# Optimization experiments

Hardware: AMD Instinct MI355X
Metric: run time of the kernel (lower is better)

## Reference

```python
import jax, jax.numpy as jnp
import numpy as np

B, T, C = 4, 2048, 1024
H, D = 16, 64  # n_heads, head_dim; C == H*D

def setup_inputs() -> dict:
    key = jax.random.key(0)
    ks = jax.random.split(key, 6)
    s_in = 1.0 / np.sqrt(C)
    x = jax.random.normal(ks[0], (B, T, C), dtype=jnp.float32)
    # causal mask: True above the diagonal -> masked to -inf
    mask = jnp.triu(jnp.ones((T, T), dtype=bool), k=1)
    Wqkv = jax.random.uniform(ks[1], (C, 3 * C), jnp.float32, -s_in, s_in)
    bqkv = jax.random.uniform(ks[2], (3 * C,), jnp.float32, -s_in, s_in)
    Wout = jax.random.uniform(ks[3], (C, C), jnp.float32, -s_in, s_in)
    bout = jax.random.uniform(ks[4], (C,), jnp.float32, -s_in, s_in)
    return {"x": x, "mask": mask, "Wqkv": Wqkv, "bqkv": bqkv, "Wout": Wout, "bout": bout}

def reference(x, mask, Wqkv, bqkv, Wout, bout):
    b, t, c = x.shape
    qkv = (x @ Wqkv + bqkv).reshape(b, t, 3, H, D)
    qkv = jnp.transpose(qkv, (2, 0, 3, 1, 4))  # [3, B, H, T, D]
    q, k, v = qkv[0], qkv[1], qkv[2]
    scores = jnp.einsum("bhqd,bhkd->bhqk", q, k) / jnp.sqrt(jnp.float32(D))
    scores = jnp.where(mask[:t, :t][None, None, :, :], -jnp.inf, scores)
    attn = jax.nn.softmax(scores, axis=-1)
    out = jnp.einsum("bhqk,bhkd->bhqd", attn, v)
    out = jnp.transpose(out, (0, 2, 1, 3)).reshape(b, t, c)
    return out @ Wout + bout
```

## Files before the change

### kernel.cpp

```cpp
#include <hip/hip_runtime.h>

typedef unsigned short u16;
typedef __attribute__((ext_vector_type(8))) short bf16x8;
typedef __attribute__((ext_vector_type(4))) short bf16x4;
typedef __attribute__((ext_vector_type(4))) float f32x4;

#define MFMA16(a, b, c) __builtin_amdgcn_mfma_f32_16x16x32_bf16(a, b, c, 0, 0, 0)

__device__ __forceinline__ u16 f2bf(float x) {
    unsigned u = __float_as_uint(x);
    return (u16)((u + 0x7fffu + ((u >> 16) & 1u)) >> 16);
}

__global__ __launch_bounds__(256) void castk(const float* __restrict__ src, u16* __restrict__ dst) {
    const int i = (blockIdx.x * 256 + threadIdx.x) * 8;
    float4 a = *(const float4*)(src + i);
    float4 b = *(const float4*)(src + i + 4);
    bf16x8 v;
    v[0] = (short)f2bf(a.x); v[1] = (short)f2bf(a.y);
    v[2] = (short)f2bf(a.z); v[3] = (short)f2bf(a.w);
    v[4] = (short)f2bf(b.x); v[5] = (short)f2bf(b.y);
    v[6] = (short)f2bf(b.z); v[7] = (short)f2bf(b.w);
    *(bf16x8*)(dst + i) = v;
}

__global__ __launch_bounds__(256) void tkern(const float* __restrict__ src, u16* __restrict__ dst,
                                             int R, int C) {
    const int tC = C >> 6;
    const int tr = (blockIdx.x / tC) << 6;
    const int tc = (blockIdx.x % tC) << 6;
    __shared__ u16 ls[64 * 68];
    const int tid = threadIdx.x;
#pragma unroll
    for (int rep = 0; rep < 2; ++rep) {
        const int f = tid * 8 + rep * 2048;
        const int r = f >> 6, c = f & 63;
        float4 a = *(const float4*)(src + (size_t)(tr + r) * C + tc + c);
        float4 b = *(const float4*)(src + (size_t)(tr + r) * C + tc + c + 4);
        bf16x4 lo, hi;
        lo[0] = (short)f2bf(a.x); lo[1] = (short)f2bf(a.y);
        lo[2] = (short)f2bf(a.z); lo[3] = (short)f2bf(a.w);
        hi[0] = (short)f2bf(b.x); hi[1] = (short)f2bf(b.y);
        hi[2] = (short)f2bf(b.z); hi[3] = (short)f2bf(b.w);
        *(bf16x4*)&ls[r * 68 + c] = lo;
        *(bf16x4*)&ls[r * 68 + c + 4] = hi;
    }
    __syncthreads();
#pragma unroll
    for (int rep = 0; rep < 2; ++rep) {
        const int f = tid * 8 + rep * 2048;
        const int rn = f >> 6, ck = f & 63;
        bf16x8 v;
#pragma unroll
        for (int j = 0; j < 8; ++j) v[j] = (short)ls[(ck + j) * 68 + rn];
        *(bf16x8*)(dst + (size_t)(tc + rn) * R + tr + ck) = v;
    }
}

template <int MODE>
__global__ __launch_bounds__(256) void gemm_k(const u16* __restrict__ A, const u16* __restrict__ Bt,
                                              const float* __restrict__ bias,
                                              u16* __restrict__ Qo, u16* __restrict__ Ko,
                                              u16* __restrict__ Vo, float* __restrict__ Of) {
    constexpr int Kd = 1024;
    const int tid = threadIdx.x;
    const int lane = tid & 63, wave = tid >> 6;
    const int wm = wave >> 1, wn = wave & 1;
    const int lr = lane & 15, lg = lane >> 4;
    const int mt = blockIdx.x & 63;
    const int nt = blockIdx.x >> 6;
    const int mbase = mt << 7, nbase = nt << 7;
    __shared__ u16 As[128 * 32];
    __shared__ u16 Bs[128 * 32];
    f32x4 acc[4][4];
#pragma unroll
    for (int i = 0; i < 4; ++i)
#pragma unroll
        for (int j = 0; j < 4; ++j) acc[i][j] = {0.f, 0.f, 0.f, 0.f};

    for (int kb = 0; kb < Kd; kb += 32) {
        __syncthreads();
#pragma unroll
        for (int rep = 0; rep < 2; ++rep) {
            const int f = tid * 8 + rep * 2048;
            const int r = f >> 5, c = f & 31;
            __builtin_amdgcn_global_load_lds(
                (const __attribute__((address_space(1))) void*)(A + (size_t)(mbase + r) * Kd + kb + c),
                (__attribute__((address_space(3))) void*)(As + f), 16, 0, 0);
            __builtin_amdgcn_global_load_lds(
                (const __attribute__((address_space(1))) void*)(Bt + (size_t)(nbase + r) * Kd + kb + c),
                (__attribute__((address_space(3))) void*)(Bs + f), 16, 0, 0);
        }
        __syncthreads();
        bf16x8 af[4], bfr[4];
#pragma unroll
        for (int i = 0; i < 4; ++i)
            af[i] = *(const bf16x8*)&As[(wm * 64 + i * 16 + lr) * 32 + lg * 8];
#pragma unroll
        for (int j = 0; j < 4; ++j)
            bfr[j] = *(const bf16x8*)&Bs[(wn * 64 + j * 16 + lr) * 32 + lg * 8];
#pragma unroll
        for (int i = 0; i < 4; ++i)
#pragma unroll
            for (int j = 0; j < 4; ++j) acc[i][j] = MFMA16(af[i], bfr[j], acc[i][j]);
    }

    const float QSCALE = 0.1803368801111137f;
#pragma unroll
    for (int j = 0; j < 4; ++j) {
        const int n = nbase + wn * 64 + j * 16 + lr;
        const float bj = bias[n];
        if (MODE == 0) {
            const int three = n >> 10;
            const int h = (n >> 6) & 15;
            const int d = n & 63;
#pragma unroll
            for (int i = 0; i < 4; ++i) {
#pragma unroll
                for (int r = 0; r < 4; ++r) {
                    const int m = mbase + wm * 64 + i * 16 + lg * 4 + r;
                    const int b = m >> 11, t = m & 2047;
                    const int bh = (b << 4) + h;
                    const float val = acc[i][j][r] + bj;
                    if (three == 0)
                        Qo[(((size_t)bh << 11) + t) * 64 + d] = f2bf(val * QSCALE);
                    else if (three == 1)
                        Ko[(((size_t)bh << 11) + t) * 64 + d] = f2bf(val);
                    else
                        Vo[(((size_t)bh << 6) + d) * 2048 + t] = f2bf(val);
                }
            }
        } else {
#pragma unroll
            for (int i = 0; i < 4; ++i) {
#pragma unroll
                for (int r = 0; r < 4; ++r) {
                    const int m = mbase + wm * 64 + i * 16 + lg * 4 + r;
                    Of[((size_t)m << 10) + n] = acc[i][j][r] + bj;
                }
            }
        }
    }
}

__global__ __launch_bounds__(256) void flash_attn(const u16* __restrict__ Q, const u16* __restrict__ Kg,
                                                  const u16* __restrict__ Vt, u16* __restrict__ Aout) {
    const int tid = threadIdx.x;
    const int lane = tid & 63, wave = tid >> 6;
    const int lr = lane & 15, lg = lane >> 4;
    const int qb = blockIdx.x;
    const int bh = blockIdx.y;
    const int b = bh >> 4, h = bh & 15;
    const size_t base = (size_t)bh << 17;

    __shared__ u16 Ks[64 * 72];
    __shared__ u16 Vs[64 * 72];
    __shared__ u16 Ps[4][16 * 72];

    const u16* Qrow = Q + base + (size_t)(qb * 64 + wave * 16 + lr) * 64;
    const bf16x8 qf0 = *(const bf16x8*)(Qrow + lg * 8);
    const bf16x8 qf1 = *(const bf16x8*)(Qrow + 32 + lg * 8);

    f32x4 o[4];
#pragma unroll
    for (int dt = 0; dt < 4; ++dt) o[dt] = {0.f, 0.f, 0.f, 0.f};
    float m_i = -INFINITY, l_i = 0.f;
    const int q_glob = qb * 64 + wave * 16 + lr;

    for (int kt = 0; kt <= qb; ++kt) {
        __syncthreads();
#pragma unroll
        for (int rep = 0; rep < 2; ++rep) {
            const int f = tid * 8 + rep * 2048;
            const int r = f >> 6, c = f & 63;
            *(bf16x8*)&Ks[r * 72 + c] = *(const bf16x8*)(Kg + base + (size_t)(kt * 64 + r) * 64 + c);
            *(bf16x8*)&Vs[r * 72 + c] = *(const bf16x8*)(Vt + base + (size_t)r * 2048 + kt * 64 + c);
        }
        __syncthreads();

        f32x4 s[4];
#pragma unroll
        for (int rt = 0; rt < 4; ++rt) {
            const bf16x8 k0 = *(const bf16x8*)&Ks[(rt * 16 + lr) * 72 + lg * 8];
            const bf16x8 k1 = *(const bf16x8*)&Ks[(rt * 16 + lr) * 72 + 32 + lg * 8];
            f32x4 z = {0.f, 0.f, 0.f, 0.f};
            z = MFMA16(k0, qf0, z);
            z = MFMA16(k1, qf1, z);
            s[rt] = z;
        }
        if (kt == qb) {
#pragma unroll
            for (int rt = 0; rt < 4; ++rt)
#pragma unroll
                for (int r = 0; r < 4; ++r) {
                    const int kv = kt * 64 + rt * 16 + lg * 4 + r;
                    if (kv > q_glob) s[rt][r] = -INFINITY;
                }
        }
        float rmax = -INFINITY;
#pragma unroll
        for (int rt = 0; rt < 4; ++rt)
#pragma unroll
            for (int r = 0; r < 4; ++r) rmax = fmaxf(rmax, s[rt][r]);
        rmax = fmaxf(rmax, __shfl_xor(rmax, 16));
        rmax = fmaxf(rmax, __shfl_xor(rmax, 32));
        const float m_new = fmaxf(m_i, rmax);
        const float alpha = exp2f(m_i - m_new);
        float rsum = 0.f;
#pragma unroll
        for (int rt = 0; rt < 4; ++rt)
#pragma unroll
            for (int r = 0; r < 4; ++r) {
                const float p = exp2f(s[rt][r] - m_new);
                s[rt][r] = p;
                rsum += p;
            }
        rsum += __shfl_xor(rsum, 16);
        rsum += __shfl_xor(rsum, 32);
        l_i = l_i * alpha + rsum;
        m_i = m_new;

#pragma unroll
        for (int rt = 0; rt < 4; ++rt) {
            bf16x4 pk;
#pragma unroll
            for (int r = 0; r < 4; ++r) pk[r] = (short)f2bf(s[rt][r]);
            *(bf16x4*)&Ps[wave][lr * 72 + rt * 16 + lg * 4] = pk;
        }
        float aq[4];
#pragma unroll
        for (int r = 0; r < 4; ++r) aq[r] = __shfl(alpha, (lane & 48) + lg * 4 + r);
#pragma unroll
        for (int dt = 0; dt < 4; ++dt)
#pragma unroll
            for (int r = 0; r < 4; ++r) o[dt][r] *= aq[r];

        const bf16x8 pf0 = *(const bf16x8*)&Ps[wave][lr * 72 + lg * 8];
        const bf16x8 pf1 = *(const bf16x8*)&Ps[wave][lr * 72 + 32 + lg * 8];
#pragma unroll
        for (int dt = 0; dt < 4; ++dt) {
            const bf16x8 v0 = *(const bf16x8*)&Vs[(dt * 16 + lr) * 72 + lg * 8];
            const bf16x8 v1 = *(const bf16x8*)&Vs[(dt * 16 + lr) * 72 + 32 + lg * 8];
            o[dt] = MFMA16(pf0, v0, o[dt]);
            o[dt] = MFMA16(pf1, v1, o[dt]);
        }
    }

    const float linv = 1.f / l_i;
    float lq[4];
#pragma unroll
    for (int r = 0; r < 4; ++r) lq[r] = __shfl(linv, (lane & 48) + lg * 4 + r);
#pragma unroll
    for (int dt = 0; dt < 4; ++dt)
#pragma unroll
        for (int r = 0; r < 4; ++r) {
            const int t = qb * 64 + wave * 16 + lg * 4 + r;
            Aout[(((size_t)(b << 11) + t) << 10) + h * 64 + dt * 16 + lr] = f2bf(o[dt][r] * lq[r]);
        }
}

extern "C" void kernel_launch(void* const* d_in, const int* in_sizes, int n_in,
                              void* d_out, int out_size, void* d_ws, size_t ws_size,
                              hipStream_t stream) {
    (void)in_sizes; (void)n_in; (void)out_size; (void)ws_size;
    const float* x    = (const float*)d_in[0];
    const float* Wqkv = (const float*)d_in[2];
    const float* bqkv = (const float*)d_in[3];
    const float* Wout = (const float*)d_in[4];
    const float* bout = (const float*)d_in[5];
    float* out = (float*)d_out;

    char* ws = (char*)d_ws;
    u16* WqkvT = (u16*)(ws);
    u16* WoutT = (u16*)(ws + 6291456);
    u16* xb    = (u16*)(ws + 8388608);
    u16* Qb    = (u16*)(ws + 25165824);
    u16* Kb    = (u16*)(ws + 41943040);
    u16* Vtb   = (u16*)(ws + 58720256);
    u16* Ab    = (u16*)(ws + 75497472);

    castk<<<dim3(4096), 256, 0, stream>>>(x, xb);
    tkern<<<dim3(16 * 48), 256, 0, stream>>>(Wqkv, WqkvT, 1024, 3072);
    tkern<<<dim3(16 * 16), 256, 0, stream>>>(Wout, WoutT, 1024, 1024);
    gemm_k<0><<<dim3(64 * 24), 256, 0, stream>>>(xb, WqkvT, bqkv, Qb, Kb, Vtb, nullptr);
    flash_attn<<<dim3(32, 64), 256, 0, stream>>>(Qb, Kb, Vtb, Ab);
    gemm_k<1><<<dim3(64 * 8), 256, 0, stream>>>(Ab, WoutT, bout, nullptr, nullptr, nullptr, out);
}
```

Before: 395.9 us.

## Pair high and low causal query blocks per workgroup to balance flash attention

Each flash-attention workgroup now handles two query tiles, block 16+bx and block 15-bx, so every workgroup does the same amount of causal work. The K/V tiles loaded into shared memory are reused by both tiles for the low block's range, which cuts global loads. The grid halves to 1024 workgroups, and each holds two sets of accumulators, which raises register pressure and may reduce occupancy. Global load addressing is also moved to precomputed pointers that are incremented each iteration.

```diff
diff --git a/kernel.cpp b/kernel.cpp
--- a/kernel.cpp
+++ b/kernel.cpp
@@ -148,36 +148,44 @@
     const int tid = threadIdx.x;
     const int lane = tid & 63, wave = tid >> 6;
     const int lr = lane & 15, lg = lane >> 4;
-    const int qb = blockIdx.x;
+    const int bx = blockIdx.x;
     const int bh = blockIdx.y;
     const int b = bh >> 4, h = bh & 15;
     const size_t base = (size_t)bh << 17;
 
+    const int qb_hi = 16 + bx;
+    const int qb_lo = 15 - bx;
+
     __shared__ u16 Ks[64 * 72];
     __shared__ u16 Vs[64 * 72];
     __shared__ u16 Ps[4][16 * 72];
 
-    const u16* Qrow = Q + base + (size_t)(qb * 64 + wave * 16 + lr) * 64;
-    const bf16x8 qf0 = *(const bf16x8*)(Qrow + lg * 8);
-    const bf16x8 qf1 = *(const bf16x8*)(Qrow + 32 + lg * 8);
-
-    f32x4 o[4];
-#pragma unroll
-    for (int dt = 0; dt < 4; ++dt) o[dt] = {0.f, 0.f, 0.f, 0.f};
-    float m_i = -INFINITY, l_i = 0.f;
-    const int q_glob = qb * 64 + wave * 16 + lr;
-
-    for (int kt = 0; kt <= qb; ++kt) {
-        __syncthreads();
-#pragma unroll
-        for (int rep = 0; rep < 2; ++rep) {
-            const int f = tid * 8 + rep * 2048;
-            const int r = f >> 6, c = f & 63;
-            *(bf16x8*)&Ks[r * 72 + c] = *(const bf16x8*)(Kg + base + (size_t)(kt * 64 + r) * 64 + c);
-            *(bf16x8*)&Vs[r * 72 + c] = *(const bf16x8*)(Vt + base + (size_t)r * 2048 + kt * 64 + c);
-        }
-        __syncthreads();
-
+    const u16* QrowH = Q + base + (size_t)(qb_hi * 64 + wave * 16 + lr) * 64;
+    const u16* QrowL = Q + base + (size_t)(qb_lo * 64 + wave * 16 + lr) * 64;
+    const bf16x8 qh0 = *(const bf16x8*)(QrowH + lg * 8);
+    const bf16x8 qh1 = *(const bf16x8*)(QrowH + 32 + lg * 8);
+    const bf16x8 ql0 = *(const bf16x8*)(QrowL + lg * 8);
+    const bf16x8 ql1 = *(const bf16x8*)(QrowL + 32 + lg * 8);
+
+    f32x4 oh[4], ol[4];
+#pragma unroll
+    for (int dt = 0; dt < 4; ++dt) { oh[dt] = {0.f, 0.f, 0.f, 0.f}; ol[dt] = {0.f, 0.f, 0.f, 0.f}; }
+    float m_hi = -INFINITY, l_hi = 0.f, m_lo = -INFINITY, l_lo = 0.f;
+    const int qg_hi = qb_hi * 64 + wave * 16 + lr;
+    const int qg_lo = qb_lo * 64 + wave * 16 + lr;
+
+    const int f0 = tid * 8, f1 = tid * 8 + 2048;
+    const u16* kp0 = Kg + base + (size_t)(f0 >> 6) * 64 + (f0 & 63);
+    const u16* kp1 = Kg + base + (size_t)(f1 >> 6) * 64 + (f1 & 63);
+    const u16* vp0 = Vt + base + (size_t)(f0 >> 6) * 2048 + (f0 & 63);
+    const u16* vp1 = Vt + base + (size_t)(f1 >> 6) * 2048 + (f1 & 63);
+    u16* ksd0 = &Ks[(f0 >> 6) * 72 + (f0 & 63)];
+    u16* ksd1 = &Ks[(f1 >> 6) * 72 + (f1 & 63)];
+    u16* vsd0 = &Vs[(f0 >> 6) * 72 + (f0 & 63)];
+    u16* vsd1 = &Vs[(f1 >> 6) * 72 + (f1 & 63)];
+
+    auto process = [&](const bf16x8& qf0, const bf16x8& qf1, f32x4* o,
+                       float& m_i, float& l_i, int q_glob, int kvbase, bool diag) {
         f32x4 s[4];
 #pragma unroll
         for (int rt = 0; rt < 4; ++rt) {
@@ -188,12 +196,12 @@
             z = MFMA16(k1, qf1, z);
             s[rt] = z;
         }
-        if (kt == qb) {
+        if (diag) {
 #pragma unroll
             for (int rt = 0; rt < 4; ++rt)
 #pragma unroll
                 for (int r = 0; r < 4; ++r) {
-                    const int kv = kt * 64 + rt * 16 + lg * 4 + r;
+                    const int kv = kvbase + rt * 16 + lg * 4 + r;
                     if (kv > q_glob) s[rt][r] = -INFINITY;
                 }
         }
@@ -244,19 +252,47 @@
             o[dt] = MFMA16(pf0, v0, o[dt]);
             o[dt] = MFMA16(pf1, v1, o[dt]);
         }
-    }
-
-    const float linv = 1.f / l_i;
-    float lq[4];
-#pragma unroll
-    for (int r = 0; r < 4; ++r) lq[r] = __shfl(linv, (lane & 48) + lg * 4 + r);
-#pragma unroll
-    for (int dt = 0; dt < 4; ++dt)
-#pragma unroll
-        for (int r = 0; r < 4; ++r) {
-            const int t = qb * 64 + wave * 16 + lg * 4 + r;
-            Aout[(((size_t)(b << 11) + t) << 10) + h * 64 + dt * 16 + lr] = f2bf(o[dt][r] * lq[r]);
-        }
+    };
+
+    for (int kt = 0; kt <= qb_hi; ++kt) {
+        __syncthreads();
+        *(bf16x8*)ksd0 = *(const bf16x8*)kp0;
+        *(bf16x8*)ksd1 = *(const bf16x8*)kp1;
+        *(bf16x8*)vsd0 = *(const bf16x8*)vp0;
+        *(bf16x8*)vsd1 = *(const bf16x8*)vp1;
+        kp0 += 4096; kp1 += 4096; vp0 += 64; vp1 += 64;
+        __syncthreads();
+
+        process(qh0, qh1, oh, m_hi, l_hi, qg_hi, kt * 64, kt == qb_hi);
+        if (kt <= qb_lo) process(ql0, ql1, ol, m_lo, l_lo, qg_lo, kt * 64, kt == qb_lo);
+    }
+
+    {
+        const float linv = 1.f / l_hi;
+        float lq[4];
+#pragma unroll
+        for (int r = 0; r < 4; ++r) lq[r] = __shfl(linv, (lane & 48) + lg * 4 + r);
+#pragma unroll
+        for (int dt = 0; dt < 4; ++dt)
+#pragma unroll
+            for (int r = 0; r < 4; ++r) {
+                const int t = qb_hi * 64 + wave * 16 + lg * 4 + r;
+                Aout[(((size_t)(b << 11) + t) << 10) + h * 64 + dt * 16 + lr] = f2bf(oh[dt][r] * lq[r]);
+            }
+    }
+    {
+        const float linv = 1.f / l_lo;
+        float lq[4];
+#pragma unroll
+        for (int r = 0; r < 4; ++r) lq[r] = __shfl(linv, (lane & 48) + lg * 4 + r);
+#pragma unroll
+        for (int dt = 0; dt < 4; ++dt)
+#pragma unroll
+            for (int r = 0; r < 4; ++r) {
+                const int t = qb_lo * 64 + wave * 16 + lg * 4 + r;
+                Aout[(((size_t)(b << 11) + t) << 10) + h * 64 + dt * 16 + lr] = f2bf(ol[dt][r] * lq[r]);
+            }
+    }
 }
 
 extern "C" void kernel_launch(void* const* d_in, const int* in_sizes, int n_in,
@@ -283,6 +319,6 @@
     tkern<<<dim3(16 * 48), 256, 0, stream>>>(Wqkv, WqkvT, 1024, 3072);
     tkern<<<dim3(16 * 16), 256, 0, stream>>>(Wout, WoutT, 1024, 1024);
     gemm_k<0><<<dim3(64 * 24), 256, 0, stream>>>(xb, WqkvT, bqkv, Qb, Kb, Vtb, nullptr);
-    flash_attn<<<dim3(32, 64), 256, 0, stream>>>(Qb, Kb, Vtb, Ab);
+    flash_attn<<<dim3(16, 64), 256, 0, stream>>>(Qb, Kb, Vtb, Ab);
     gemm_k<1><<<dim3(64 * 8), 256, 0, stream>>>(Ab, WoutT, bout, nullptr, nullptr, nullptr, out);
 }
```

Result: faster. 340.7 us (-13.9%).

## Pair causal query blocks per workgroup and load K/V fragments directly into registers

Applied to the files above, without the earlier changes.

The flash-attention kernel now assigns each 128-thread workgroup a high and a low query block (16+bx and 15-bx), so every workgroup does roughly the same causal work. Each wave handles 32 query rows across both blocks and reads K/V fragments straight from global memory into registers, dropping the LDS staging and __syncthreads. This balances the triangular workload and reuses each K/V tile for four query subtiles, at the cost of much higher register pressure and uncoalesced per-lane global loads. P is also rounded to bf16 with a cheaper round-half-up conversion instead of round-to-nearest-even.

```diff
diff --git a/kernel.cpp b/kernel.cpp
--- a/kernel.cpp
+++ b/kernel.cpp
@@ -10,6 +10,9 @@
 __device__ __forceinline__ u16 f2bf(float x) {
     unsigned u = __float_as_uint(x);
     return (u16)((u + 0x7fffu + ((u >> 16) & 1u)) >> 16);
+}
+__device__ __forceinline__ u16 f2bf_fast(float x) {
+    return (u16)((__float_as_uint(x) + 0x8000u) >> 16);
 }
 
 __global__ __launch_bounds__(256) void castk(const float* __restrict__ src, u16* __restrict__ dst) {
@@ -143,120 +146,150 @@
     }
 }
 
-__global__ __launch_bounds__(256) void flash_attn(const u16* __restrict__ Q, const u16* __restrict__ Kg,
-                                                  const u16* __restrict__ Vt, u16* __restrict__ Aout) {
+__global__ __launch_bounds__(128, 2) void flash_attn(const u16* __restrict__ Q, const u16* __restrict__ Kg,
+                                                     const u16* __restrict__ Vt, u16* __restrict__ Aout) {
     const int tid = threadIdx.x;
     const int lane = tid & 63, wave = tid >> 6;
     const int lr = lane & 15, lg = lane >> 4;
-    const int qb = blockIdx.x;
+    const int bx = blockIdx.x;
     const int bh = blockIdx.y;
     const int b = bh >> 4, h = bh & 15;
     const size_t base = (size_t)bh << 17;
 
-    __shared__ u16 Ks[64 * 72];
-    __shared__ u16 Vs[64 * 72];
-    __shared__ u16 Ps[4][16 * 72];
-
-    const u16* Qrow = Q + base + (size_t)(qb * 64 + wave * 16 + lr) * 64;
-    const bf16x8 qf0 = *(const bf16x8*)(Qrow + lg * 8);
-    const bf16x8 qf1 = *(const bf16x8*)(Qrow + 32 + lg * 8);
-
-    f32x4 o[4];
-#pragma unroll
-    for (int dt = 0; dt < 4; ++dt) o[dt] = {0.f, 0.f, 0.f, 0.f};
-    float m_i = -INFINITY, l_i = 0.f;
-    const int q_glob = qb * 64 + wave * 16 + lr;
-
-    for (int kt = 0; kt <= qb; ++kt) {
-        __syncthreads();
-#pragma unroll
-        for (int rep = 0; rep < 2; ++rep) {
-            const int f = tid * 8 + rep * 2048;
-            const int r = f >> 6, c = f & 63;
-            *(bf16x8*)&Ks[r * 72 + c] = *(const bf16x8*)(Kg + base + (size_t)(kt * 64 + r) * 64 + c);
-            *(bf16x8*)&Vs[r * 72 + c] = *(const bf16x8*)(Vt + base + (size_t)r * 2048 + kt * 64 + c);
-        }
-        __syncthreads();
-
-        f32x4 s[4];
+    const int qb_hi = 16 + bx;
+    const int qb_lo = 15 - bx;
+
+    __shared__ u16 Ps[2][16 * 72];
+
+    int qbase[4];
+    qbase[0] = qb_hi * 64 + wave * 32;
+    qbase[1] = qbase[0] + 16;
+    qbase[2] = qb_lo * 64 + wave * 32;
+    qbase[3] = qbase[2] + 16;
+
+    bf16x8 qf[4][2];
+#pragma unroll
+    for (int st = 0; st < 4; ++st) {
+        const u16* p = Q + base + (size_t)(qbase[st] + lr) * 64;
+        qf[st][0] = *(const bf16x8*)(p + lg * 8);
+        qf[st][1] = *(const bf16x8*)(p + 32 + lg * 8);
+    }
+
+    f32x4 o[4][4];
+#pragma unroll
+    for (int st = 0; st < 4; ++st)
+#pragma unroll
+        for (int dt = 0; dt < 4; ++dt) o[st][dt] = {0.f, 0.f, 0.f, 0.f};
+    float m_[4] = {-INFINITY, -INFINITY, -INFINITY, -INFINITY};
+    float l_[4] = {0.f, 0.f, 0.f, 0.f};
+
+    const u16* Kbase = Kg + base + (size_t)lr * 64 + lg * 8;
+    const u16* Vbase = Vt + base + (size_t)lr * 2048 + lg * 8;
+
+    for (int kt = 0; kt <= qb_hi; ++kt) {
+        bf16x8 kf[4][2], vf[4][2];
+        const u16* kp = Kbase + (size_t)kt * 4096;
 #pragma unroll
         for (int rt = 0; rt < 4; ++rt) {
-            const bf16x8 k0 = *(const bf16x8*)&Ks[(rt * 16 + lr) * 72 + lg * 8];
-            const bf16x8 k1 = *(const bf16x8*)&Ks[(rt * 16 + lr) * 72 + 32 + lg * 8];
-            f32x4 z = {0.f, 0.f, 0.f, 0.f};
-            z = MFMA16(k0, qf0, z);
-            z = MFMA16(k1, qf1, z);
-            s[rt] = z;
-        }
-        if (kt == qb) {
+            kf[rt][0] = *(const bf16x8*)(kp + rt * 1024);
+            kf[rt][1] = *(const bf16x8*)(kp + rt * 1024 + 32);
+        }
+        const u16* vp = Vbase + kt * 64;
+#pragma unroll
+        for (int dt = 0; dt < 4; ++dt) {
+            vf[dt][0] = *(const bf16x8*)(vp + dt * 32768);
+            vf[dt][1] = *(const bf16x8*)(vp + dt * 32768 + 32);
+        }
+
+        auto process = [&](int st, bool diag) {
+            f32x4 s[4];
+#pragma unroll
+            for (int rt = 0; rt < 4; ++rt) {
+                f32x4 z = {0.f, 0.f, 0.f, 0.f};
+                z = MFMA16(kf[rt][0], qf[st][0], z);
+                z = MFMA16(kf[rt][1], qf[st][1], z);
+                s[rt] = z;
+            }
+            if (diag) {
+                const int q_glob = qbase[st] + lr;
+#pragma unroll
+                for (int rt = 0; rt < 4; ++rt)
+#pragma unroll
+                    for (int r = 0; r < 4; ++r) {
+                        const int kv = kt * 64 + rt * 16 + lg * 4 + r;
+                        if (kv > q_glob) s[rt][r] = -INFINITY;
+                    }
+            }
+            float rmax = -INFINITY;
 #pragma unroll
             for (int rt = 0; rt < 4; ++rt)
 #pragma unroll
+                for (int r = 0; r < 4; ++r) rmax = fmaxf(rmax, s[rt][r]);
+            rmax = fmaxf(rmax, __shfl_xor(rmax, 16));
+            rmax = fmaxf(rmax, __shfl_xor(rmax, 32));
+            const float m_new = fmaxf(m_[st], rmax);
+            const float alpha = exp2f(m_[st] - m_new);
+            float rsum = 0.f;
+#pragma unroll
+            for (int rt = 0; rt < 4; ++rt)
+#pragma unroll
                 for (int r = 0; r < 4; ++r) {
-                    const int kv = kt * 64 + rt * 16 + lg * 4 + r;
-                    if (kv > q_glob) s[rt][r] = -INFINITY;
+                    const float p = exp2f(s[rt][r] - m_new);
+                    s[rt][r] = p;
+                    rsum += p;
                 }
-        }
-        float rmax = -INFINITY;
-#pragma unroll
-        for (int rt = 0; rt < 4; ++rt)
-#pragma unroll
-            for (int r = 0; r < 4; ++r) rmax = fmaxf(rmax, s[rt][r]);
-        rmax = fmaxf(rmax, __shfl_xor(rmax, 16));
-        rmax = fmaxf(rmax, __shfl_xor(rmax, 32));
-        const float m_new = fmaxf(m_i, rmax);
-        const float alpha = exp2f(m_i - m_new);
-        float rsum = 0.f;
-#pragma unroll
-        for (int rt = 0; rt < 4; ++rt)
+            rsum += __shfl_xor(rsum, 16);
+            rsum += __shfl_xor(rsum, 32);
+            l_[st] = l_[st] * alpha + rsum;
+            m_[st] = m_new;
+
+#pragma unroll
+            for (int rt = 0; rt < 4; ++rt) {
+                bf16x4 pk;
+#pragma unroll
+                for (int r = 0; r < 4; ++r) pk[r] = (short)f2bf_fast(s[rt][r]);
+                *(bf16x4*)&Ps[wave][lr * 72 + rt * 16 + lg * 4] = pk;
+            }
+            float aq[4];
+#pragma unroll
+            for (int r = 0; r < 4; ++r) aq[r] = __shfl(alpha, (lane & 48) + lg * 4 + r);
+#pragma unroll
+            for (int dt = 0; dt < 4; ++dt)
+#pragma unroll
+                for (int r = 0; r < 4; ++r) o[st][dt][r] *= aq[r];
+
+            const bf16x8 pf0 = *(const bf16x8*)&Ps[wave][lr * 72 + lg * 8];
+            const bf16x8 pf1 = *(const bf16x8*)&Ps[wave][lr * 72 + 32 + lg * 8];
+#pragma unroll
+            for (int dt = 0; dt < 4; ++dt) {
+                o[st][dt] = MFMA16(pf0, vf[dt][0], o[st][dt]);
+                o[st][dt] = MFMA16(pf1, vf[dt][1], o[st][dt]);
+            }
+        };
+
+        process(0, kt == qb_hi);
+        process(1, kt == qb_hi);
+        if (kt <= qb_lo) {
+            process(2, kt == qb_lo);
+            process(3, kt == qb_lo);
+        }
+    }
+
+#pragma unroll
+    for (int st = 0; st < 4; ++st) {
+        const float linv = 1.f / l_[st];
+        float lq[4];
+#pragma unroll
+        for (int r = 0; r < 4; ++r) lq[r] = __shfl(linv, (lane & 48) + lg * 4 + r);
+#pragma unroll
+        for (int dt = 0; dt < 4; ++dt)
 #pragma unroll
             for (int r = 0; r < 4; ++r) {
-                const float p = exp2f(s[rt][r] - m_new);
-                s[rt][r] = p;
-                rsum += p;
-            }
-        rsum += __shfl_xor(rsum, 16);
-        rsum += __shfl_xor(rsum, 32);
-        l_i = l_i * alpha + rsum;
-        m_i = m_new;
-
-#pragma unroll
-        for (int rt = 0; rt < 4; ++rt) {
-            bf16x4 pk;
-#pragma unroll
-            for (int r = 0; r < 4; ++r) pk[r] = (short)f2bf(s[rt][r]);
-            *(bf16x4*)&Ps[wave][lr * 72 + rt * 16 + lg * 4] = pk;
-        }
-        float aq[4];
-#pragma unroll
-        for (int r = 0; r < 4; ++r) aq[r] = __shfl(alpha, (lane & 48) + lg * 4 + r);
-#pragma unroll
-        for (int dt = 0; dt < 4; ++dt)
-#pragma unroll
-            for (int r = 0; r < 4; ++r) o[dt][r] *= aq[r];
-
-        const bf16x8 pf0 = *(const bf16x8*)&Ps[wave][lr * 72 + lg * 8];
-        const bf16x8 pf1 = *(const bf16x8*)&Ps[wave][lr * 72 + 32 + lg * 8];
-#pragma unroll
-        for (int dt = 0; dt < 4; ++dt) {
-            const bf16x8 v0 = *(const bf16x8*)&Vs[(dt * 16 + lr) * 72 + lg * 8];
-            const bf16x8 v1 = *(const bf16x8*)&Vs[(dt * 16 + lr) * 72 + 32 + lg * 8];
-            o[dt] = MFMA16(pf0, v0, o[dt]);
-            o[dt] = MFMA16(pf1, v1, o[dt]);
-        }
-    }
-
-    const float linv = 1.f / l_i;
-    float lq[4];
-#pragma unroll
-    for (int r = 0; r < 4; ++r) lq[r] = __shfl(linv, (lane & 48) + lg * 4 + r);
-#pragma unroll
-    for (int dt = 0; dt < 4; ++dt)
-#pragma unroll
-        for (int r = 0; r < 4; ++r) {
-            const int t = qb * 64 + wave * 16 + lg * 4 + r;
-            Aout[(((size_t)(b << 11) + t) << 10) + h * 64 + dt * 16 + lr] = f2bf(o[dt][r] * lq[r]);
-        }
+                const int t = qbase[st] + lg * 4 + r;
+                Aout[(((size_t)(b << 11) + t) << 10) + h * 64 + dt * 16 + lr] =
+                    f2bf(o[st][dt][r] * lq[r]);
+            }
+    }
 }
 
 extern "C" void kernel_launch(void* const* d_in, const int* in_sizes, int n_in,
@@ -283,6 +316,6 @@
     tkern<<<dim3(16 * 48), 256, 0, stream>>>(Wqkv, WqkvT, 1024, 3072);
     tkern<<<dim3(16 * 16), 256, 0, stream>>>(Wout, WoutT, 1024, 1024);
     gemm_k<0><<<dim3(64 * 24), 256, 0, stream>>>(xb, WqkvT, bqkv, Qb, Kb, Vtb, nullptr);
-    flash_attn<<<dim3(32, 64), 256, 0, stream>>>(Qb, Kb, Vtb, Ab);
+    flash_attn<<<dim3(16, 64), 128, 0, stream>>>(Qb, Kb, Vtb, Ab);
     gemm_k<1><<<dim3(64 * 8), 256, 0, stream>>>(Ab, WoutT, bout, nullptr, nullptr, nullptr, out);
 }
```

New measurement: 336.9 us. -14.9%, faster.
